# Kernel tuning notes

Measured on AMD Instinct MI355X. Metric: run time of the kernel, lower is better.

The kernel has to match this reference:

```python
import jax, jax.numpy as jnp
import numpy as np

EPS = 1e-12  # F.normalize default eps
TEMPERATURE = 1.0


def _l2_normalize(x):
    n = jnp.sqrt(jnp.sum(x * x, axis=-1, keepdims=True))
    return x / jnp.maximum(n, EPS)


def setup_inputs() -> dict:
    key = jax.random.key(0)
    k1, k2 = jax.random.split(key)
    B, C, H, W = 16, 256, 128, 256
    K = 19
    features = jax.random.normal(k1, (B, C, H, W), dtype=jnp.float32)
    prototypes = jax.random.normal(k2, (K, C), dtype=jnp.float32)
    distance_scale = jnp.ones((1,), dtype=jnp.float32)
    return {"features": features, "prototypes": prototypes,
            "distance_scale": distance_scale}


def reference(features, prototypes, distance_scale):
    B, C, H, W = features.shape
    K = prototypes.shape[0]
    # [B,C,H,W] -> [B*H*W, C]
    x = features.transpose(0, 2, 3, 1).reshape(-1, C)
    xn = _l2_normalize(x)            # [N, C]
    pn = _l2_normalize(prototypes)   # [K, C]
    # pairwise Euclidean distance via the stable quadratic expansion
    # ||a-b||^2 = ||a||^2 + ||b||^2 - 2 a.b  (norms ~1 after normalization)
    xx = jnp.sum(xn * xn, axis=-1)   # [N]
    pp = jnp.sum(pn * pn, axis=-1)   # [K]
    d2 = xx[:, None] + pp[None, :] - 2.0 * jnp.einsum('nc,kc->nk', xn, pn)
    dist = jnp.sqrt(jnp.maximum(d2, 0.0))  # [N, K]
    dist = jnp.abs(distance_scale) * dist
    logits = -dist.reshape(B, H, W, K).transpose(0, 3, 1, 2)  # [B,K,H,W]
    return logits / TEMPERATURE
```

## Files before the change

kernel.cpp:

```cpp
#include <hip/hip_runtime.h>


typedef float f4 __attribute__((ext_vector_type(4)));

namespace {
constexpr int kC     = 256;
constexpr int kK     = 19;
constexpr int kKP    = 20;
constexpr int kHW    = 128 * 256;
constexpr int kBlock = 256;
constexpr int kPix   = 4;
constexpr int kUnroll= 8;
}

__global__ void proto_norm_kernel(const float* __restrict__ proto,
                                  float* __restrict__ pn,
                                  float* __restrict__ pp)
{
    const int tid  = threadIdx.x;
    const int lane = tid & 63;
    const int wv   = tid >> 6;
    for (int k = wv; k < kK; k += 4) {
        float v[4];
        float ss = 0.f;
        #pragma unroll
        for (int j = 0; j < 4; ++j) {
            v[j] = proto[k * kC + j * 64 + lane];
            ss = fmaf(v[j], v[j], ss);
        }
        #pragma unroll
        for (int m = 1; m < 64; m <<= 1)
            ss += __shfl_xor(ss, m, 64);
        const float inv = 1.0f / fmaxf(sqrtf(ss), 1e-12f);
        #pragma unroll
        for (int j = 0; j < 4; ++j)
            pn[(j * 64 + lane) * kKP + k] = v[j] * inv;
        if (lane == 0) pp[k] = ss * inv * inv;
    }
    if (tid < kC) pn[tid * kKP + kK] = 0.f;
}

__global__ __launch_bounds__(kBlock, 2)
void isomax_main(const float* __restrict__ feat,
                 const float* __restrict__ pn,
                 const float* __restrict__ pp,
                 const float* __restrict__ dscale,
                 float* __restrict__ out)
{
    const int tid  = threadIdx.x;
    const int gpix = (blockIdx.x * kBlock + tid) * kPix;
    const int b    = gpix >> 15;
    const int hw   = gpix & (kHW - 1);
    const float* fp = feat + (size_t)b * kC * kHW + hw;

    float xx[4] = {0.f, 0.f, 0.f, 0.f};
    f4 dot[kK];
    #pragma unroll
    for (int k = 0; k < kK; ++k) dot[k] = (f4)(0.f);

    for (int cc = 0; cc < kC; cc += kUnroll) {
        f4 v[kUnroll];
        #pragma unroll
        for (int u = 0; u < kUnroll; ++u)
            v[u] = __builtin_nontemporal_load(
                       (const f4*)(fp + (size_t)(cc + u) * kHW));
        #pragma unroll
        for (int u = 0; u < kUnroll; ++u) {
            const int c = cc + u;
            const f4* __restrict__ prow = (const f4*)(pn + (size_t)c * kKP);
            f4 P[5];
            #pragma unroll
            for (int q = 0; q < 5; ++q) P[q] = prow[q];
            const float* p = (const float*)P;
            xx[0] = fmaf(v[u].x, v[u].x, xx[0]);
            xx[1] = fmaf(v[u].y, v[u].y, xx[1]);
            xx[2] = fmaf(v[u].z, v[u].z, xx[2]);
            xx[3] = fmaf(v[u].w, v[u].w, xx[3]);
            #pragma unroll
            for (int k = 0; k < kK; ++k) {
                dot[k].x = fmaf(p[k], v[u].x, dot[k].x);
                dot[k].y = fmaf(p[k], v[u].y, dot[k].y);
                dot[k].z = fmaf(p[k], v[u].z, dot[k].z);
                dot[k].w = fmaf(p[k], v[u].w, dot[k].w);
            }
        }
    }

    float inv[4], xnsq[4];
    #pragma unroll
    for (int j = 0; j < 4; ++j) {
        inv[j]  = 1.0f / fmaxf(sqrtf(xx[j]), 1e-12f);
        xnsq[j] = xx[j] * inv[j] * inv[j];
    }
    const float sc = fabsf(dscale[0]);

    float* op = out + (size_t)b * kK * kHW + hw;
    #pragma unroll
    for (int k = 0; k < kK; ++k) {
        const float ppk = pp[k];
        f4 o;
        o.x = -sc * sqrtf(fmaxf(xnsq[0] + ppk - 2.0f * dot[k].x * inv[0], 0.f));
        o.y = -sc * sqrtf(fmaxf(xnsq[1] + ppk - 2.0f * dot[k].y * inv[1], 0.f));
        o.z = -sc * sqrtf(fmaxf(xnsq[2] + ppk - 2.0f * dot[k].z * inv[2], 0.f));
        o.w = -sc * sqrtf(fmaxf(xnsq[3] + ppk - 2.0f * dot[k].w * inv[3], 0.f));
        __builtin_nontemporal_store(o, (f4*)(op + (size_t)k * kHW));
    }
}

extern "C" void kernel_launch(void* const* d_in, const int* in_sizes, int n_in,
                              void* d_out, int out_size, void* d_ws, size_t ws_size,
                              hipStream_t stream) {
    const float* feat   = (const float*)d_in[0];
    const float* proto  = (const float*)d_in[1];
    const float* dscale = (const float*)d_in[2];
    float* out = (float*)d_out;

    float* pn = (float*)d_ws;
    float* pp = pn + kC * kKP;

    proto_norm_kernel<<<dim3(1), dim3(256), 0, stream>>>(proto, pn, pp);

    const int npix    = in_sizes[0] / kC;
    const int threads = npix / kPix;
    isomax_main<<<dim3(threads / kBlock), dim3(kBlock), 0, stream>>>(
        feat, pn, pp, dscale, out);
}
```

Before: 695.3 us.

## Halve pixels per thread and double-buffer channel loads for more occupancy

```diff
diff --git a/kernel.cpp b/kernel.cpp
--- a/kernel.cpp
+++ b/kernel.cpp
@@ -1,6 +1,7 @@
 #include <hip/hip_runtime.h>
 
 
+typedef float f2 __attribute__((ext_vector_type(2)));
 typedef float f4 __attribute__((ext_vector_type(4)));
 
 namespace {
@@ -9,8 +10,8 @@
 constexpr int kKP    = 20;
 constexpr int kHW    = 128 * 256;
 constexpr int kBlock = 256;
-constexpr int kPix   = 4;
-constexpr int kUnroll= 8;
+constexpr int kPix   = 2;
+constexpr int kU     = 8;
 }
 
 __global__ void proto_norm_kernel(const float* __restrict__ proto,
@@ -40,7 +41,7 @@
     if (tid < kC) pn[tid * kKP + kK] = 0.f;
 }
 
-__global__ __launch_bounds__(kBlock, 2)
+__global__ __launch_bounds__(kBlock, 4)
 void isomax_main(const float* __restrict__ feat,
                  const float* __restrict__ pn,
                  const float* __restrict__ pp,
@@ -53,42 +54,65 @@
     const int hw   = gpix & (kHW - 1);
     const float* fp = feat + (size_t)b * kC * kHW + hw;
 
-    float xx[4] = {0.f, 0.f, 0.f, 0.f};
-    f4 dot[kK];
+    float xx[kPix] = {0.f, 0.f};
+    f2 dot[kK];
     #pragma unroll
-    for (int k = 0; k < kK; ++k) dot[k] = (f4)(0.f);
+    for (int k = 0; k < kK; ++k) dot[k] = (f2)(0.f);
 
-    for (int cc = 0; cc < kC; cc += kUnroll) {
-        f4 v[kUnroll];
+    f2 bufA[kU], bufB[kU];
+
+    #pragma unroll
+    for (int u = 0; u < kU; ++u)
+        bufA[u] = __builtin_nontemporal_load((const f2*)(fp + (size_t)u * kHW));
+
+    for (int cc = 0; cc < kC; cc += 2 * kU) {
         #pragma unroll
-        for (int u = 0; u < kUnroll; ++u)
-            v[u] = __builtin_nontemporal_load(
-                       (const f4*)(fp + (size_t)(cc + u) * kHW));
+        for (int u = 0; u < kU; ++u)
+            bufB[u] = __builtin_nontemporal_load(
+                          (const f2*)(fp + (size_t)(cc + kU + u) * kHW));
         #pragma unroll
-        for (int u = 0; u < kUnroll; ++u) {
+        for (int u = 0; u < kU; ++u) {
             const int c = cc + u;
             const f4* __restrict__ prow = (const f4*)(pn + (size_t)c * kKP);
             f4 P[5];
             #pragma unroll
             for (int q = 0; q < 5; ++q) P[q] = prow[q];
             const float* p = (const float*)P;
-            xx[0] = fmaf(v[u].x, v[u].x, xx[0]);
-            xx[1] = fmaf(v[u].y, v[u].y, xx[1]);
-            xx[2] = fmaf(v[u].z, v[u].z, xx[2]);
-            xx[3] = fmaf(v[u].w, v[u].w, xx[3]);
+            xx[0] = fmaf(bufA[u].x, bufA[u].x, xx[0]);
+            xx[1] = fmaf(bufA[u].y, bufA[u].y, xx[1]);
             #pragma unroll
             for (int k = 0; k < kK; ++k) {
-                dot[k].x = fmaf(p[k], v[u].x, dot[k].x);
-                dot[k].y = fmaf(p[k], v[u].y, dot[k].y);
-                dot[k].z = fmaf(p[k], v[u].z, dot[k].z);
-                dot[k].w = fmaf(p[k], v[u].w, dot[k].w);
+                dot[k].x = fmaf(p[k], bufA[u].x, dot[k].x);
+                dot[k].y = fmaf(p[k], bufA[u].y, dot[k].y);
+            }
+        }
+        if (cc + 2 * kU < kC) {
+            #pragma unroll
+            for (int u = 0; u < kU; ++u)
+                bufA[u] = __builtin_nontemporal_load(
+                              (const f2*)(fp + (size_t)(cc + 2 * kU + u) * kHW));
+        }
+        #pragma unroll
+        for (int u = 0; u < kU; ++u) {
+            const int c = cc + kU + u;
+            const f4* __restrict__ prow = (const f4*)(pn + (size_t)c * kKP);
+            f4 P[5];
+            #pragma unroll
+            for (int q = 0; q < 5; ++q) P[q] = prow[q];
+            const float* p = (const float*)P;
+            xx[0] = fmaf(bufB[u].x, bufB[u].x, xx[0]);
+            xx[1] = fmaf(bufB[u].y, bufB[u].y, xx[1]);
+            #pragma unroll
+            for (int k = 0; k < kK; ++k) {
+                dot[k].x = fmaf(p[k], bufB[u].x, dot[k].x);
+                dot[k].y = fmaf(p[k], bufB[u].y, dot[k].y);
             }
         }
     }
 
-    float inv[4], xnsq[4];
+    float inv[kPix], xnsq[kPix];
     #pragma unroll
-    for (int j = 0; j < 4; ++j) {
+    for (int j = 0; j < kPix; ++j) {
         inv[j]  = 1.0f / fmaxf(sqrtf(xx[j]), 1e-12f);
         xnsq[j] = xx[j] * inv[j] * inv[j];
     }
@@ -98,12 +122,10 @@
     #pragma unroll
     for (int k = 0; k < kK; ++k) {
         const float ppk = pp[k];
-        f4 o;
+        f2 o;
         o.x = -sc * sqrtf(fmaxf(xnsq[0] + ppk - 2.0f * dot[k].x * inv[0], 0.f));
         o.y = -sc * sqrtf(fmaxf(xnsq[1] + ppk - 2.0f * dot[k].y * inv[1], 0.f));
-        o.z = -sc * sqrtf(fmaxf(xnsq[2] + ppk - 2.0f * dot[k].z * inv[2], 0.f));
-        o.w = -sc * sqrtf(fmaxf(xnsq[3] + ppk - 2.0f * dot[k].w * inv[3], 0.f));
-        __builtin_nontemporal_store(o, (f4*)(op + (size_t)k * kHW));
+        __builtin_nontemporal_store(o, (f2*)(op + (size_t)k * kHW));
     }
 }
 
```

Result: slower. 785.1 us (+12.9%).
